# Optimization experiments

Hardware: AMD Instinct MI355X
Metric: run time of the kernel (lower is better)

The kernel has to match this reference:

```python
import jax, jax.numpy as jnp
import numpy as np

ALPHA = 0.1  # dt/tau = 10/100


def setup_inputs() -> dict:
    key = jax.random.key(0)
    k1, k2, k3 = jax.random.split(key, 3)
    seq_len, batch, in_dim, hid = 1024, 64, 128, 512
    inp = jax.random.normal(k1, (seq_len, batch, in_dim), dtype=jnp.float32)
    W_in = jax.random.normal(k2, (hid, in_dim), dtype=jnp.float32) / np.sqrt(in_dim)
    b_in = jnp.zeros((hid,), dtype=jnp.float32)
    W_hid = jax.random.normal(k3, (hid, hid), dtype=jnp.float32) / np.sqrt(hid)
    b_hid = jnp.zeros((hid,), dtype=jnp.float32)
    return {"input": inp, "W_in": W_in, "b_in": b_in, "W_hid": W_hid, "b_hid": b_hid}


def reference(input, W_in, b_in, W_hid, b_hid):
    # leaky RNN: v_t = (1-a) v_{t-1} + a (W_hid fr_{t-1} + b_hid + W_in u_t + b_in)
    #            fr_t = relu(v_t)
    hid = W_hid.shape[0]
    batch = input.shape[1]
    # precompute input projection for all steps: (seq, batch, hid)
    u_proj = jnp.einsum('sbi,hi->sbh', input, W_in) + b_in

    v0 = jnp.zeros((batch, hid), dtype=input.dtype)
    fr0 = jax.nn.relu(v0)

    def step(carry, u_t):
        fr, v = carry
        v = (1.0 - ALPHA) * v + ALPHA * (fr @ W_hid.T + b_hid + u_t)
        fr = jax.nn.relu(v)
        return (fr, v), fr

    _, states = jax.lax.scan(step, (fr0, v0), u_proj)
    return states  # (seq_len, batch, hidden)
```

## Files before the change

kernel.cpp:

```cpp
#include <hip/hip_runtime.h>
#include <hip/hip_bf16.h>
#include <stdint.h>


#define SEQ   1024
#define BATCH 64
#define INDIM 128
#define HID   512
#define HG    16
#define BGN   4

typedef __attribute__((ext_vector_type(8))) short   short8;
typedef __attribute__((ext_vector_type(4))) float   floatx4;
typedef unsigned long long ull;

__device__ __forceinline__ unsigned short f2bf(float x) {
  union { float f; unsigned int u; } v; v.f = x;
  unsigned int r = v.u + 0x7fffu + ((v.u >> 16) & 1u);
  return (unsigned short)(r >> 16);
}
__device__ __forceinline__ ull pack4(unsigned short a, unsigned short b,
                                     unsigned short c, unsigned short d) {
  return (ull)a | ((ull)b << 16) | ((ull)c << 32) | ((ull)d << 48);
}

#define TA_SB 64
#define TA_H  128
#define TA_K  64
#define APAD  65

__global__ __launch_bounds__(256) void uproj_kernel(
    const float* __restrict__ inp, const float* __restrict__ Win,
    const float* __restrict__ bin, float* __restrict__ out)
{
  __shared__ float sIn[TA_SB * APAD];
  __shared__ float sW [TA_H  * APAD];
  const int tid = threadIdx.x;
  const int sb0 = (blockIdx.x >> 2) * TA_SB;
  const int h0  = (blockIdx.x & 3) * TA_H;
  const int tx = tid & 15, ty = tid >> 4;

  float acc[4][8];
  #pragma unroll
  for (int i = 0; i < 4; ++i)
    #pragma unroll
    for (int j = 0; j < 8; ++j) acc[i][j] = 0.f;

  for (int kt = 0; kt < INDIM / TA_K; ++kt) {
    #pragma unroll
    for (int p = 0; p < 4; ++p) {
      int idx = tid + 256 * p;
      int row = idx >> 4, c4 = (idx & 15) << 2;
      const float4 v = *(const float4*)(inp + (size_t)(sb0 + row) * INDIM + kt * TA_K + c4);
      float* d = sIn + row * APAD + c4;
      d[0] = v.x; d[1] = v.y; d[2] = v.z; d[3] = v.w;
    }
    #pragma unroll
    for (int p = 0; p < 8; ++p) {
      int idx = tid + 256 * p;
      int row = idx >> 4, c4 = (idx & 15) << 2;
      const float4 v = *(const float4*)(Win + (size_t)(h0 + row) * INDIM + kt * TA_K + c4);
      float* d = sW + row * APAD + c4;
      d[0] = v.x; d[1] = v.y; d[2] = v.z; d[3] = v.w;
    }
    __syncthreads();

    for (int k = 0; k < TA_K; ++k) {
      float a[4], b[8];
      #pragma unroll
      for (int i = 0; i < 4; ++i) a[i] = sIn[(ty + 16 * i) * APAD + k];
      #pragma unroll
      for (int j = 0; j < 8; ++j) b[j] = sW[(tx + 16 * j) * APAD + k];
      #pragma unroll
      for (int i = 0; i < 4; ++i)
        #pragma unroll
        for (int j = 0; j < 8; ++j) acc[i][j] = fmaf(a[i], b[j], acc[i][j]);
    }
    __syncthreads();
  }

  #pragma unroll
  for (int j = 0; j < 8; ++j) {
    float bb = bin[h0 + tx + 16 * j];
    #pragma unroll
    for (int i = 0; i < 4; ++i)
      out[(size_t)(sb0 + ty + 16 * i) * HID + h0 + tx + 16 * j] = acc[i][j] + bb;
  }
}

__global__ __launch_bounds__(64) void scan_kernel(
    const float* __restrict__ Whid, const float* __restrict__ bhid,
    float* __restrict__ uo,
    ull* __restrict__ frA)
{
  const int lane = threadIdx.x & 63;
  const int bid  = blockIdx.x;
  const int bg = bid >> 5;
  const int hg = (bid >> 1) & 15;
  const int w  = bid & 1;
  const int b0 = bg * 16;
  const int m  = lane & 15;
  const int q  = lane >> 4;
  const int n0 = hg * 32 + w * 16 + q * 4;
  const int na = hg * 32 + w * 16 + m;

  short8 aw[HG];
  {
    const float* wrow = Whid + (size_t)na * HID + q * 8;
    #pragma unroll
    for (int kk = 0; kk < HG; ++kk) {
      const float4 a = *(const float4*)(wrow + kk * 32);
      const float4 b = *(const float4*)(wrow + kk * 32 + 4);
      union { unsigned short s[8]; short8 v; } u;
      u.s[0] = f2bf(a.x); u.s[1] = f2bf(a.y); u.s[2] = f2bf(a.z); u.s[3] = f2bf(a.w);
      u.s[4] = f2bf(b.x); u.s[5] = f2bf(b.y); u.s[6] = f2bf(b.z); u.s[7] = f2bf(b.w);
      aw[kk] = u.v;
    }
  }
  const floatx4 bias4 = *(const floatx4*)(bhid + n0);

  const ull MASKT = 0x8000800080008000ull;
  float v[4] = {0.f, 0.f, 0.f, 0.f};
  const float OMA = 0.9f, AL = 0.1f;

  for (int t = 0; t < SEQ; ++t) {
    const floatx4 uu = *(const floatx4*)(uo + ((size_t)t * BATCH + b0 + m) * HID + n0);

    floatx4 acc[4];
    #pragma unroll
    for (int j = 0; j < 4; ++j) acc[j] = (floatx4){0.f, 0.f, 0.f, 0.f};

    if (t > 0) {
      const int slot = (t - 1) & 1;
      const ull expv = (((t - 1) >> 1) & 1) ? MASKT : 0ull;
      const ull* ap = frA + (size_t)(slot * BGN + bg) * HG * 128
                          + (size_t)(2 * q) * 16 + m;
      ull lo[HG], hi[HG];
      for (;;) {
        int ok = 1;
        #pragma unroll
        for (int kk = 0; kk < HG; ++kk) {
          lo[kk] = __hip_atomic_load(ap + (size_t)kk * 128,
                                     __ATOMIC_RELAXED, __HIP_MEMORY_SCOPE_AGENT);
          hi[kk] = __hip_atomic_load(ap + (size_t)kk * 128 + 16,
                                     __ATOMIC_RELAXED, __HIP_MEMORY_SCOPE_AGENT);
          ok &= (int)(((lo[kk] & MASKT) == expv) & ((hi[kk] & MASKT) == expv));
        }
        if (__all(ok)) break;
      }
      #pragma unroll
      for (int kk = 0; kk < HG; ++kk) {
        union { ull u[2]; short8 s; } bf;
        bf.u[0] = lo[kk] & ~MASKT;
        bf.u[1] = hi[kk] & ~MASKT;
        acc[kk & 3] = __builtin_amdgcn_mfma_f32_16x16x32_bf16(aw[kk], bf.s,
                                                              acc[kk & 3], 0, 0, 0);
      }
    }

    float fr[4];
    #pragma unroll
    for (int r = 0; r < 4; ++r) {
      float s = acc[0][r] + acc[1][r] + acc[2][r] + acc[3][r];
      v[r] = OMA * v[r] + AL * (s + bias4[r] + uu[r]);
      fr[r] = fmaxf(v[r], 0.f);
    }

    {
      ull pk = pack4(f2bf(fr[0]), f2bf(fr[1]), f2bf(fr[2]), f2bf(fr[3]));
      if ((t >> 1) & 1) pk |= MASKT;
      ull* dst = frA + (size_t)(((t & 1) * BGN + bg) * HG + hg) * 128
                     + (size_t)(w * 4 + q) * 16 + m;
      __hip_atomic_store(dst, pk, __ATOMIC_RELAXED, __HIP_MEMORY_SCOPE_AGENT);
    }

    *(floatx4*)(uo + ((size_t)t * BATCH + b0 + m) * HID + n0) =
        (floatx4){fr[0], fr[1], fr[2], fr[3]};
  }
}

extern "C" void kernel_launch(void* const* d_in, const int* in_sizes, int n_in,
                              void* d_out, int out_size, void* d_ws, size_t ws_size,
                              hipStream_t stream) {
  const float* inp  = (const float*)d_in[0];
  const float* Win  = (const float*)d_in[1];
  const float* bin  = (const float*)d_in[2];
  const float* Whid = (const float*)d_in[3];
  const float* bhid = (const float*)d_in[4];
  float* out = (float*)d_out;

  ull* frA = (ull*)d_ws;

  uproj_kernel<<<dim3((65536 / TA_SB) * (HID / TA_H)), dim3(256), 0, stream>>>(
      inp, Win, bin, out);
  scan_kernel<<<dim3(BGN * HG * 2), dim3(64), 0, stream>>>(
      Whid, bhid, out, frA);
}
```

Before: 2.152 ms.

## Prefetch input projections in batches, fold hidden bias, remap blocks across XCDs

Moves b_hid into the input-projection epilogue so the scan no longer loads and adds it. The scan now prefetches eight timesteps of projected input into registers with nontemporal loads, taking the per-step global load off the serial dependency chain. Blocks are remapped over a grid of 256 with half of them exiting immediately, so each batch group lands on its own XCD under round-robin dispatch and cross-block flag polling stays within a shared L2. This costs more registers per lane, and it depends on a particular block-to-XCD assignment.

After: 3.674 ms. 1.71x slower.

```diff
diff --git a/kernel.cpp b/kernel.cpp
--- a/kernel.cpp
+++ b/kernel.cpp
@@ -31,7 +31,8 @@
 
 __global__ __launch_bounds__(256) void uproj_kernel(
     const float* __restrict__ inp, const float* __restrict__ Win,
-    const float* __restrict__ bin, float* __restrict__ out)
+    const float* __restrict__ bin, const float* __restrict__ bhid,
+    float* __restrict__ out)
 {
   __shared__ float sIn[TA_SB * APAD];
   __shared__ float sW [TA_H  * APAD];
@@ -81,7 +82,7 @@
 
   #pragma unroll
   for (int j = 0; j < 8; ++j) {
-    float bb = bin[h0 + tx + 16 * j];
+    float bb = bin[h0 + tx + 16 * j] + bhid[h0 + tx + 16 * j];
     #pragma unroll
     for (int i = 0; i < 4; ++i)
       out[(size_t)(sb0 + ty + 16 * i) * HID + h0 + tx + 16 * j] = acc[i][j] + bb;
@@ -89,15 +90,18 @@
 }
 
 __global__ __launch_bounds__(64) void scan_kernel(
-    const float* __restrict__ Whid, const float* __restrict__ bhid,
+    const float* __restrict__ Whid,
     float* __restrict__ uo,
     ull* __restrict__ frA)
 {
   const int lane = threadIdx.x & 63;
   const int bid  = blockIdx.x;
-  const int bg = bid >> 5;
-  const int hg = (bid >> 1) & 15;
-  const int w  = bid & 1;
+  const int sl   = bid & 7;
+  if (sl >= BGN) return;
+  const int bg  = sl;
+  const int idx = bid >> 3;
+  const int hg  = idx & 15;
+  const int w   = idx >> 4;
   const int b0 = bg * 16;
   const int m  = lane & 15;
   const int q  = lane >> 4;
@@ -117,65 +121,85 @@
       aw[kk] = u.v;
     }
   }
-  const floatx4 bias4 = *(const floatx4*)(bhid + n0);
 
   const ull MASKT = 0x8000800080008000ull;
   float v[4] = {0.f, 0.f, 0.f, 0.f};
   const float OMA = 0.9f, AL = 0.1f;
 
-  for (int t = 0; t < SEQ; ++t) {
-    const floatx4 uu = *(const floatx4*)(uo + ((size_t)t * BATCH + b0 + m) * HID + n0);
-
-    floatx4 acc[4];
-    #pragma unroll
-    for (int j = 0; j < 4; ++j) acc[j] = (floatx4){0.f, 0.f, 0.f, 0.f};
-
-    if (t > 0) {
-      const int slot = (t - 1) & 1;
-      const ull expv = (((t - 1) >> 1) & 1) ? MASKT : 0ull;
-      const ull* ap = frA + (size_t)(slot * BGN + bg) * HG * 128
-                          + (size_t)(2 * q) * 16 + m;
-      ull lo[HG], hi[HG];
-      for (;;) {
-        int ok = 1;
+  const float* ubase = uo + (size_t)(b0 + m) * HID + n0;
+  const size_t tstride = (size_t)BATCH * HID;
+
+  floatx4 ub[8];
+  #pragma unroll
+  for (int j = 0; j < 8; ++j)
+    ub[j] = __builtin_nontemporal_load((const floatx4*)(ubase + (size_t)j * tstride));
+
+  for (int tb = 0; tb < SEQ; tb += 8) {
+    #pragma unroll
+    for (int j = 0; j < 8; ++j) {
+      const int t = tb + j;
+      const floatx4 uu = ub[j];
+
+      floatx4 acc[4];
+      #pragma unroll
+      for (int a = 0; a < 4; ++a) acc[a] = (floatx4){0.f, 0.f, 0.f, 0.f};
+
+      if (t > 0) {
+        const int slot = (t - 1) & 1;
+        const ull expv = (((t - 1) >> 1) & 1) ? MASKT : 0ull;
+        const ull* ap = frA + (size_t)(slot * BGN + bg) * HG * 128
+                            + (size_t)(2 * q) * 16 + m;
+        ull lo[HG], hi[HG];
+        for (;;) {
+          int ok = 1;
+          #pragma unroll
+          for (int kk = 0; kk < HG; ++kk) {
+            lo[kk] = __hip_atomic_load(ap + (size_t)kk * 128,
+                                       __ATOMIC_RELAXED, __HIP_MEMORY_SCOPE_AGENT);
+            hi[kk] = __hip_atomic_load(ap + (size_t)kk * 128 + 16,
+                                       __ATOMIC_RELAXED, __HIP_MEMORY_SCOPE_AGENT);
+            ok &= (int)(((lo[kk] & MASKT) == expv) & ((hi[kk] & MASKT) == expv));
+          }
+          if (__all(ok)) break;
+        }
         #pragma unroll
         for (int kk = 0; kk < HG; ++kk) {
-          lo[kk] = __hip_atomic_load(ap + (size_t)kk * 128,
-                                     __ATOMIC_RELAXED, __HIP_MEMORY_SCOPE_AGENT);
-          hi[kk] = __hip_atomic_load(ap + (size_t)kk * 128 + 16,
-                                     __ATOMIC_RELAXED, __HIP_MEMORY_SCOPE_AGENT);
-          ok &= (int)(((lo[kk] & MASKT) == expv) & ((hi[kk] & MASKT) == expv));
+          union { ull u[2]; short8 s; } bf;
+          bf.u[0] = lo[kk] & ~MASKT;
+          bf.u[1] = hi[kk] & ~MASKT;
+          acc[kk & 3] = __builtin_amdgcn_mfma_f32_16x16x32_bf16(aw[kk], bf.s,
+                                                                acc[kk & 3], 0, 0, 0);
         }
-        if (__all(ok)) break;
-      }
-      #pragma unroll
-      for (int kk = 0; kk < HG; ++kk) {
-        union { ull u[2]; short8 s; } bf;
-        bf.u[0] = lo[kk] & ~MASKT;
-        bf.u[1] = hi[kk] & ~MASKT;
-        acc[kk & 3] = __builtin_amdgcn_mfma_f32_16x16x32_bf16(aw[kk], bf.s,
-                                                              acc[kk & 3], 0, 0, 0);
-      }
-    }
-
-    float fr[4];
-    #pragma unroll
-    for (int r = 0; r < 4; ++r) {
-      float s = acc[0][r] + acc[1][r] + acc[2][r] + acc[3][r];
-      v[r] = OMA * v[r] + AL * (s + bias4[r] + uu[r]);
-      fr[r] = fmaxf(v[r], 0.f);
-    }
-
-    {
-      ull pk = pack4(f2bf(fr[0]), f2bf(fr[1]), f2bf(fr[2]), f2bf(fr[3]));
-      if ((t >> 1) & 1) pk |= MASKT;
-      ull* dst = frA + (size_t)(((t & 1) * BGN + bg) * HG + hg) * 128
-                     + (size_t)(w * 4 + q) * 16 + m;
-      __hip_atomic_store(dst, pk, __ATOMIC_RELAXED, __HIP_MEMORY_SCOPE_AGENT);
-    }
-
-    *(floatx4*)(uo + ((size_t)t * BATCH + b0 + m) * HID + n0) =
-        (floatx4){fr[0], fr[1], fr[2], fr[3]};
+      }
+
+      float fr[4];
+      #pragma unroll
+      for (int r = 0; r < 4; ++r) {
+        float s = acc[0][r] + acc[1][r] + acc[2][r] + acc[3][r];
+        v[r] = OMA * v[r] + AL * (s + uu[r]);
+        fr[r] = fmaxf(v[r], 0.f);
+      }
+
+      {
+        ull pk = pack4(f2bf(fr[0]), f2bf(fr[1]), f2bf(fr[2]), f2bf(fr[3]));
+        if ((t >> 1) & 1) pk |= MASKT;
+        ull* dst = frA + (size_t)(((t & 1) * BGN + bg) * HG + hg) * 128
+                       + (size_t)(w * 4 + q) * 16 + m;
+        __hip_atomic_store(dst, pk, __ATOMIC_RELAXED, __HIP_MEMORY_SCOPE_AGENT);
+      }
+
+      *(floatx4*)(uo + (size_t)t * tstride + (size_t)(b0 + m) * HID + n0) =
+          (floatx4){fr[0], fr[1], fr[2], fr[3]};
+
+      if (j == 7 && tb + 8 < SEQ) {
+        #pragma unroll
+        for (int jj = 0; jj < 8; ++jj) {
+          const int tn = tb + 8 + jj;
+          ub[jj] = __builtin_nontemporal_load(
+              (const floatx4*)(ubase + (size_t)(tn < SEQ ? tn : SEQ - 1) * tstride));
+        }
+      }
+    }
   }
 }
 
@@ -192,7 +216,7 @@
   ull* frA = (ull*)d_ws;
 
   uproj_kernel<<<dim3((65536 / TA_SB) * (HID / TA_H)), dim3(256), 0, stream>>>(
-      inp, Win, bin, out);
-  scan_kernel<<<dim3(BGN * HG * 2), dim3(64), 0, stream>>>(
-      Whid, bhid, out, frA);
-}
+      inp, Win, bin, bhid, out);
+  scan_kernel<<<dim3(256), dim3(64), 0, stream>>>(
+      Whid, out, frA);
+}
```
